# Optimization experiments

Hardware: AMD Instinct MI355X
Metric: run time of the kernel (lower is better)

## Reference

```python
import jax, jax.numpy as jnp
import numpy as np

B, C, H, W, K = 16, 64, 192, 192, 3

def setup_inputs() -> dict:
    key = jax.random.key(0)
    k1, k2, k3, k4 = jax.random.split(key, 4)
    x = jax.random.normal(k1, (B, C, H, W), dtype=jnp.float32)
    DoT = jax.random.uniform(k2, (B,), dtype=jnp.float32)
    W0 = jax.random.normal(k3, (C, C, K, K), dtype=jnp.float32) * 0.05
    W1 = jax.random.normal(k4, (C, C, K, K), dtype=jnp.float32) * 0.05
    return {"x": x, "DoT": DoT, "W0": W0, "W1": W1}

def reference(x, DoT, W0, W1):
    # Per-sample blended kernels: [B, C_o, C_i, K, K]
    d = DoT[:, None, None, None, None]
    kernel = (1.0 - d) * W0[None] + d * W1[None]

    def conv_one(xi, ki):
        # xi: [C_i, H, W], ki: [C_o, C_i, K, K]
        out = jax.lax.conv_general_dilated(
            xi[None], ki,
            window_strides=(1, 1),
            padding=((1, 1), (1, 1)),
            dimension_numbers=("NCHW", "OIHW", "NCHW"),
        )
        return out[0]

    y = jax.vmap(conv_one)(x, kernel)  # [B, C_o, H, W]
    return y
```

## Files before the change

kernel.cpp:

```cpp
#include <hip/hip_runtime.h>
#include <hip/hip_bf16.h>
#include <stdint.h>

#define NB 16
#define NC 64
#define NH 192
#define NW 192
#define NKDIM 576

typedef __bf16 bf16x8 __attribute__((ext_vector_type(8)));
typedef __bf16 bf16x4 __attribute__((ext_vector_type(4)));
typedef float  f32x4  __attribute__((ext_vector_type(4)));

static __device__ __forceinline__ __bf16 f2bf(float f) { return (__bf16)f; }

__global__ __launch_bounds__(256)
void blend_kernel(const float* __restrict__ W0, const float* __restrict__ W1,
                  const float* __restrict__ DoT, __bf16* __restrict__ A) {
    int idx = blockIdx.x * 256 + threadIdx.x;
    int k   = idx % NKDIM;
    int co  = (idx / NKDIM) % NC;
    int b   = idx / (NKDIM * NC);
    int tap = k >> 6;
    int ci  = k & 63;
    float d  = DoT[b];
    int wi   = (co * NC + ci) * 9 + tap;
    float v  = (1.0f - d) * W0[wi] + d * W1[wi];
    A[idx] = f2bf(v);
}

__global__ __launch_bounds__(256)
void nhwc_cvt_kernel(const float* __restrict__ x, __bf16* __restrict__ xt) {
    __shared__ float tile[64 * 68];

    const int b  = blockIdx.z;
    const int h  = blockIdx.y;
    const int wt = blockIdx.x * 64;
    const int t  = threadIdx.x;

    {
        const int ci = t & 63;
        const int wq = t >> 6;
        const float* src = x + ((size_t)(b * NC + ci) * NH + h) * NW + wt;
        #pragma unroll
        for (int w4l = 0; w4l < 4; ++w4l) {
            const int w4 = wq * 4 + w4l;
            f32x4 v = *(const f32x4*)(src + w4 * 4);
            #pragma unroll
            for (int j = 0; j < 4; ++j)
                tile[(w4 * 4 + j) * 68 + ci] = v[j];
        }
    }
    __syncthreads();

    __bf16* dst = xt + ((size_t)(b * NH + h) * NW + wt) * NC;
    #pragma unroll
    for (int it = 0; it < 2; ++it) {
        const int c   = it * 256 + t;
        const int w   = c >> 3;
        const int cig = c & 7;
        f32x4 v0 = *(const f32x4*)&tile[w * 68 + cig * 8];
        f32x4 v1 = *(const f32x4*)&tile[w * 68 + cig * 8 + 4];
        bf16x8 pk = { f2bf(v0[0]), f2bf(v0[1]), f2bf(v0[2]), f2bf(v0[3]),
                      f2bf(v1[0]), f2bf(v1[1]), f2bf(v1[2]), f2bf(v1[3]) };
        *(bf16x8*)(dst + (size_t)w * NC + cig * 8) = pk;
    }
}

__global__ __launch_bounds__(512, 4)
void conv_nhwc_kernel(const __bf16* __restrict__ xt, const __bf16* __restrict__ A,
                      float* __restrict__ out) {
    __shared__ __bf16 xs[4 * 66 * 8 * 8];

    const int b  = blockIdx.z;
    const int h0 = blockIdx.y * 2;
    const int w0 = blockIdx.x * 64;

    const int tid  = threadIdx.x;
    const int lane = tid & 63;
    const int wave = tid >> 6;

    {
        #pragma unroll
        for (int it = 0; it < 4; ++it) {
            const int c   = it * 512 + tid;
            const int r   = c / 528;
            const int rem = c - r * 528;
            const int w   = rem >> 3;
            const int g   = rem & 7;
            const int gr  = h0 - 1 + r;
            const int gw  = w0 - 1 + w;
            const bool ok = (gr >= 0) && (gr < NH) && (gw >= 0) && (gw < NW);
            bf16x8 v = {};
            if (ok)
                v = *(const bf16x8*)(xt + ((size_t)(b * NH + gr) * NW + gw) * NC + g * 8);
            *(bf16x8*)&xs[(((r * 66 + w) * 8) + (g ^ (w & 7))) * 8] = v;
        }
        if (tid < 64) {
            const int c   = 2048 + tid;
            const int r   = 3;
            const int rem = c - 3 * 528;
            const int w   = rem >> 3;
            const int g   = rem & 7;
            const int gr  = h0 + 2;
            const int gw  = w0 - 1 + w;
            const bool ok = (gr < NH) && (gw < NW);
            bf16x8 v = {};
            if (ok)
                v = *(const bf16x8*)(xt + ((size_t)(b * NH + gr) * NW + gw) * NC + g * 8);
            *(bf16x8*)&xs[(((r * 66 + w) * 8) + (g ^ (w & 7))) * 8] = v;
        }
    }

    const int mt   = wave & 3;
    const int nh   = wave >> 2;
    const int n    = lane & 15;
    const int quad = lane >> 4;

    const __bf16* Ap = A + ((size_t)b * NC + mt * 16 + n) * NKDIM + quad * 8;
    bf16x8 afr[9][2];
    #pragma unroll
    for (int tap = 0; tap < 9; ++tap)
        #pragma unroll
        for (int ch = 0; ch < 2; ++ch)
            afr[tap][ch] = *(const bf16x8*)(Ap + tap * 64 + ch * 32);

    __syncthreads();

    f32x4 acc[4];
    #pragma unroll
    for (int nt = 0; nt < 4; ++nt) acc[nt] = (f32x4){0.f, 0.f, 0.f, 0.f};

    #pragma unroll
    for (int tap = 0; tap < 9; ++tap) {
        const int dh  = tap / 3;
        const int dw  = tap - dh * 3;
        const int row = nh + dh;
        #pragma unroll
        for (int ch = 0; ch < 2; ++ch) {
            #pragma unroll
            for (int nt = 0; nt < 4; ++nt) {
                const int wl = dw + nt * 16 + n;
                const int gp = (ch * 4 + quad) ^ (wl & 7);
                bf16x8 bfr = *(const bf16x8*)&xs[(((row * 66 + wl) * 8) + gp) * 8];
                acc[nt] = __builtin_amdgcn_mfma_f32_16x16x32_bf16(
                    afr[tap][ch], bfr, acc[nt], 0, 0, 0);
            }
        }
    }

    const int h = h0 + nh;
    float* ob = out + (size_t)b * NC * NH * NW + (size_t)h * NW + w0;
    #pragma unroll
    for (int reg = 0; reg < 4; ++reg) {
        const int co = mt * 16 + quad * 4 + reg;
        float* orow = ob + (size_t)co * NH * NW;
        #pragma unroll
        for (int nt = 0; nt < 4; ++nt) {
            orow[nt * 16 + n] = acc[nt][reg];
        }
    }
}

__global__ __launch_bounds__(512, 4)
void conv_nchw_kernel(const float* __restrict__ x, const __bf16* __restrict__ A,
                      float* __restrict__ out) {
    __shared__ __bf16 xs[4 * 66 * 72];

    const int b  = blockIdx.z;
    const int h0 = blockIdx.y * 2;
    const int w0 = blockIdx.x * 64;

    const int tid  = threadIdx.x;
    const int lane = tid & 63;
    const int wave = tid >> 6;

    {
        const int r  = tid >> 7;
        const int s  = tid & 127;
        const int gr = h0 - 1 + r;
        const bool rowok = (gr >= 0) && (gr < NH);
        const float* xb = x + (size_t)b * NC * NH * NW + (ptrdiff_t)gr * NW;

        #pragma unroll
        for (int j = 0; j < 8; ++j) {
            const int p   = j * 128 + s;
            const int wl  = p & 63;
            const int ci4 = p >> 6;
            const int gw  = w0 - 1 + wl;
            const bool ok = rowok && (gw >= 0);
            float v0 = ok ? xb[(size_t)(ci4 * 4 + 0) * NH * NW + gw] : 0.0f;
            float v1 = ok ? xb[(size_t)(ci4 * 4 + 1) * NH * NW + gw] : 0.0f;
            float v2 = ok ? xb[(size_t)(ci4 * 4 + 2) * NH * NW + gw] : 0.0f;
            float v3 = ok ? xb[(size_t)(ci4 * 4 + 3) * NH * NW + gw] : 0.0f;
            bf16x4 pk = { f2bf(v0), f2bf(v1), f2bf(v2), f2bf(v3) };
            const int g  = ci4 >> 1;
            const int gp = g ^ ((wl >> 3) & 7);
            *(bf16x4*)&xs[(r * 66 + wl) * 72 + gp * 8 + (ci4 & 1) * 4] = pk;
        }
        if (s < 32) {
            const int wl  = 64 + (s & 1);
            const int ci4 = s >> 1;
            const int gw  = w0 - 1 + wl;
            const bool ok = rowok && (gw < NW);
            float v0 = ok ? xb[(size_t)(ci4 * 4 + 0) * NH * NW + gw] : 0.0f;
            float v1 = ok ? xb[(size_t)(ci4 * 4 + 1) * NH * NW + gw] : 0.0f;
            float v2 = ok ? xb[(size_t)(ci4 * 4 + 2) * NH * NW + gw] : 0.0f;
            float v3 = ok ? xb[(size_t)(ci4 * 4 + 3) * NH * NW + gw] : 0.0f;
            bf16x4 pk = { f2bf(v0), f2bf(v1), f2bf(v2), f2bf(v3) };
            const int g  = ci4 >> 1;
            const int gp = g ^ ((wl >> 3) & 7);
            *(bf16x4*)&xs[(r * 66 + wl) * 72 + gp * 8 + (ci4 & 1) * 4] = pk;
        }
    }

    const int mt   = wave & 3;
    const int nh   = wave >> 2;
    const int n    = lane & 15;
    const int quad = lane >> 4;

    const __bf16* Ap = A + ((size_t)b * NC + mt * 16 + n) * NKDIM + quad * 8;
    bf16x8 afr[9][2];
    #pragma unroll
    for (int tap = 0; tap < 9; ++tap)
        #pragma unroll
        for (int ch = 0; ch < 2; ++ch)
            afr[tap][ch] = *(const bf16x8*)(Ap + tap * 64 + ch * 32);

    __syncthreads();

    f32x4 acc[4];
    #pragma unroll
    for (int nt = 0; nt < 4; ++nt) acc[nt] = (f32x4){0.f, 0.f, 0.f, 0.f};

    #pragma unroll
    for (int tap = 0; tap < 9; ++tap) {
        const int dh  = tap / 3;
        const int dw  = tap - dh * 3;
        const int row = nh + dh;
        #pragma unroll
        for (int ch = 0; ch < 2; ++ch) {
            const int g = ch * 4 + quad;
            #pragma unroll
            for (int nt = 0; nt < 4; ++nt) {
                const int wl = dw + nt * 16 + n;
                const int gp = g ^ ((wl >> 3) & 7);
                bf16x8 bfr = *(const bf16x8*)&xs[(row * 66 + wl) * 72 + gp * 8];
                acc[nt] = __builtin_amdgcn_mfma_f32_16x16x32_bf16(
                    afr[tap][ch], bfr, acc[nt], 0, 0, 0);
            }
        }
    }

    const int h = h0 + nh;
    float* ob = out + (size_t)b * NC * NH * NW + (size_t)h * NW + w0;
    #pragma unroll
    for (int reg = 0; reg < 4; ++reg) {
        const int co = mt * 16 + quad * 4 + reg;
        float* orow = ob + (size_t)co * NH * NW;
        #pragma unroll
        for (int nt = 0; nt < 4; ++nt) {
            orow[nt * 16 + n] = acc[nt][reg];
        }
    }
}

extern "C" void kernel_launch(void* const* d_in, const int* in_sizes, int n_in,
                              void* d_out, int out_size, void* d_ws, size_t ws_size,
                              hipStream_t stream) {
    const float* x   = (const float*)d_in[0];
    const float* DoT = (const float*)d_in[1];
    const float* W0  = (const float*)d_in[2];
    const float* W1  = (const float*)d_in[3];
    float* out = (float*)d_out;

    const size_t A_BYTES  = (size_t)NB * NC * NKDIM * 2;
    const size_t XT_BYTES = (size_t)NB * NH * NW * NC * 2;
    __bf16* A  = (__bf16*)d_ws;
    __bf16* xt = (__bf16*)((char*)d_ws + A_BYTES);

    blend_kernel<<<dim3((NB * NC * NKDIM) / 256), 256, 0, stream>>>(W0, W1, DoT, A);

    if (ws_size >= A_BYTES + XT_BYTES) {
        nhwc_cvt_kernel<<<dim3(NW / 64, NH, NB), dim3(256), 0, stream>>>(x, xt);
        conv_nhwc_kernel<<<dim3(NW / 64, NH / 2, NB), dim3(512), 0, stream>>>(xt, A, out);
    } else {
        conv_nchw_kernel<<<dim3(NW / 64, NH / 2, NB), dim3(512), 0, stream>>>(x, A, out);
    }
}
```

Before: 373.5 us.

## Transpose NHWC convert via padded scalar LDS and prefetch A fragments per tap

The NCHW-to-NHWC conversion now reads coalesced along W for each channel. It stages the data in a 65-stride LDS tile and gathers eight channels per thread with scalar LDS reads, in place of vector reads from a 68-stride tile. The conv kernel no longer preloads all 18 A fragments into registers. It keeps only the current tap's two fragments and prefetches the next tap's, which lowers register pressure at the cost of global loads inside the MFMA loop. The MFMA ordering is also interleaved per output tile.

After: 346.3 us. 7.3% less time.

```diff
diff --git a/kernel.cpp b/kernel.cpp
--- a/kernel.cpp
+++ b/kernel.cpp
@@ -31,7 +31,7 @@
 
 __global__ __launch_bounds__(256)
 void nhwc_cvt_kernel(const float* __restrict__ x, __bf16* __restrict__ xt) {
-    __shared__ float tile[64 * 68];
+    __shared__ float tile[64 * 65];
 
     const int b  = blockIdx.z;
     const int h  = blockIdx.y;
@@ -39,17 +39,12 @@
     const int t  = threadIdx.x;
 
     {
-        const int ci = t & 63;
-        const int wq = t >> 6;
-        const float* src = x + ((size_t)(b * NC + ci) * NH + h) * NW + wt;
-        #pragma unroll
-        for (int w4l = 0; w4l < 4; ++w4l) {
-            const int w4 = wq * 4 + w4l;
-            f32x4 v = *(const f32x4*)(src + w4 * 4);
-            #pragma unroll
-            for (int j = 0; j < 4; ++j)
-                tile[(w4 * 4 + j) * 68 + ci] = v[j];
-        }
+        const int w   = t & 63;
+        const int ciq = t >> 6;
+        const float* src = x + ((size_t)(b * NC + ciq * 16) * NH + h) * NW + wt + w;
+        #pragma unroll
+        for (int j = 0; j < 16; ++j)
+            tile[(ciq * 16 + j) * 65 + w] = src[(size_t)j * NH * NW];
     }
     __syncthreads();
 
@@ -59,10 +54,16 @@
         const int c   = it * 256 + t;
         const int w   = c >> 3;
         const int cig = c & 7;
-        f32x4 v0 = *(const f32x4*)&tile[w * 68 + cig * 8];
-        f32x4 v1 = *(const f32x4*)&tile[w * 68 + cig * 8 + 4];
-        bf16x8 pk = { f2bf(v0[0]), f2bf(v0[1]), f2bf(v0[2]), f2bf(v0[3]),
-                      f2bf(v1[0]), f2bf(v1[1]), f2bf(v1[2]), f2bf(v1[3]) };
+        float v0 = tile[(cig * 8 + 0) * 65 + w];
+        float v1 = tile[(cig * 8 + 1) * 65 + w];
+        float v2 = tile[(cig * 8 + 2) * 65 + w];
+        float v3 = tile[(cig * 8 + 3) * 65 + w];
+        float v4 = tile[(cig * 8 + 4) * 65 + w];
+        float v5 = tile[(cig * 8 + 5) * 65 + w];
+        float v6 = tile[(cig * 8 + 6) * 65 + w];
+        float v7 = tile[(cig * 8 + 7) * 65 + w];
+        bf16x8 pk = { f2bf(v0), f2bf(v1), f2bf(v2), f2bf(v3),
+                      f2bf(v4), f2bf(v5), f2bf(v6), f2bf(v7) };
         *(bf16x8*)(dst + (size_t)w * NC + cig * 8) = pk;
     }
 }
@@ -118,35 +119,37 @@
     const int quad = lane >> 4;
 
     const __bf16* Ap = A + ((size_t)b * NC + mt * 16 + n) * NKDIM + quad * 8;
-    bf16x8 afr[9][2];
-    #pragma unroll
-    for (int tap = 0; tap < 9; ++tap)
-        #pragma unroll
-        for (int ch = 0; ch < 2; ++ch)
-            afr[tap][ch] = *(const bf16x8*)(Ap + tap * 64 + ch * 32);
+    bf16x8 a0 = *(const bf16x8*)(Ap + 0);
+    bf16x8 a1 = *(const bf16x8*)(Ap + 32);
+
+    f32x4 acc[4];
+    #pragma unroll
+    for (int nt = 0; nt < 4; ++nt) acc[nt] = (f32x4){0.f, 0.f, 0.f, 0.f};
 
     __syncthreads();
 
-    f32x4 acc[4];
-    #pragma unroll
-    for (int nt = 0; nt < 4; ++nt) acc[nt] = (f32x4){0.f, 0.f, 0.f, 0.f};
-
     #pragma unroll
     for (int tap = 0; tap < 9; ++tap) {
+        const int tn = (tap < 8) ? tap + 1 : 8;
+        const bf16x8 na0 = *(const bf16x8*)(Ap + tn * 64);
+        const bf16x8 na1 = *(const bf16x8*)(Ap + tn * 64 + 32);
+
         const int dh  = tap / 3;
         const int dw  = tap - dh * 3;
         const int row = nh + dh;
         #pragma unroll
-        for (int ch = 0; ch < 2; ++ch) {
-            #pragma unroll
-            for (int nt = 0; nt < 4; ++nt) {
-                const int wl = dw + nt * 16 + n;
-                const int gp = (ch * 4 + quad) ^ (wl & 7);
-                bf16x8 bfr = *(const bf16x8*)&xs[(((row * 66 + wl) * 8) + gp) * 8];
-                acc[nt] = __builtin_amdgcn_mfma_f32_16x16x32_bf16(
-                    afr[tap][ch], bfr, acc[nt], 0, 0, 0);
-            }
-        }
+        for (int nt = 0; nt < 4; ++nt) {
+            const int wl = dw + nt * 16 + n;
+            const int sw = wl & 7;
+            const int base = ((row * 66 + wl) * 8) * 8;
+            bf16x8 b0 = *(const bf16x8*)&xs[base + ((0 * 4 + quad) ^ sw) * 8];
+            acc[nt] = __builtin_amdgcn_mfma_f32_16x16x32_bf16(
+                a0, b0, acc[nt], 0, 0, 0);
+            bf16x8 b1 = *(const bf16x8*)&xs[base + ((1 * 4 + quad) ^ sw) * 8];
+            acc[nt] = __builtin_amdgcn_mfma_f32_16x16x32_bf16(
+                a1, b1, acc[nt], 0, 0, 0);
+        }
+        a0 = na0; a1 = na1;
     }
 
     const int h = h0 + nh;
```
